# Performance work log

Measured on AMD Instinct MI355X. Metric: run time of the kernel, lower is better.

The kernel has to match this reference:

```python
import jax, jax.numpy as jnp
import numpy as np

B, C, L, MID, HID, OUT, K = 4096, 6, 1024, 512, 512, 256, 5
EPS = 1e-5


def _bn_eval(x, g, b, m, v):
    # BatchNorm1d eval mode on (B, C, T): normalize per channel with running stats
    inv = g / jnp.sqrt(v + EPS)
    return (x - m[None, :, None]) * inv[None, :, None] + b[None, :, None]


def setup_inputs() -> dict:
    key = jax.random.key(0)
    ks = jax.random.split(key, 12)
    s_in = 1.0 / np.sqrt(L)
    s_hid = 1.0 / np.sqrt(HID)
    inp = {
        "x": jax.random.normal(ks[0], (B, C, L), jnp.float32),
        # k stacked self-attention branches (two Linear(L, MID) each)
        "aW1": jax.random.normal(ks[1], (K, L, MID), jnp.float32) * s_in,
        "ab1": jnp.zeros((K, MID), jnp.float32),
        "aW2": jax.random.normal(ks[2], (K, L, MID), jnp.float32) * s_in,
        "ab2": jnp.zeros((K, MID), jnp.float32),
        # linearExchangeLayer: Linear(K*C, C)
        "linW": jax.random.normal(ks[3], (K * C, C), jnp.float32) / np.sqrt(K * C),
        "linb": jnp.zeros((C,), jnp.float32),
        # GraphConvolution weights
        "gW1": jax.random.normal(ks[4], (L, HID), jnp.float32) * s_in,
        "gb1": jnp.zeros((HID,), jnp.float32),
        "gW2": jax.random.normal(ks[5], (HID, OUT), jnp.float32) * s_hid,
        "gb2": jnp.zeros((OUT,), jnp.float32),
        # PReLU (single shared parameter, torch default 0.25)
        "prelu_a": jnp.array(0.25, jnp.float32),
        # BatchNorm1d params + running stats (eval mode)
        "bn1_g": jnp.ones((C,), jnp.float32),
        "bn1_b": jnp.zeros((C,), jnp.float32),
        "bn1_m": jnp.zeros((C,), jnp.float32),
        "bn1_v": jnp.ones((C,), jnp.float32),
        "bn2_g": jnp.ones((C,), jnp.float32),
        "bn2_b": jnp.zeros((C,), jnp.float32),
        "bn2_m": jnp.zeros((C,), jnp.float32),
        "bn2_v": jnp.ones((C,), jnp.float32),
    }
    return inp


def reference(x, aW1, ab1, aW2, ab2, linW, linb, gW1, gb1, gW2, gb2,
              prelu_a, bn1_g, bn1_b, bn1_m, bn1_v, bn2_g, bn2_b, bn2_m, bn2_v):
    b, c, l = x.shape
    k = aW1.shape[0]
    # --- multi-head attention adjacency: (b, c, c) ---
    q = jnp.einsum('bcl,klm->bkcm', x, aW1) + ab1[None, :, None, :]
    kv = jnp.einsum('bcl,klm->bkcm', x, aW2) + ab2[None, :, None, :]
    scores = jax.nn.softmax(jnp.einsum('bkcm,bkdm->bkcd', q, kv), axis=-1)
    # concat heads along last dim: (b, c, k*c)
    cat = scores.transpose(0, 2, 1, 3).reshape(b, c, k * c)
    A = jax.nn.softmax(cat @ linW + linb, axis=-1)  # (b, c, c)
    # --- GraphConvolution 1 (dropout identity in eval) ---
    h = jnp.einsum('bcd,bdh->bch', A, x @ gW1) + gb1
    # PReLU then BatchNorm1d
    h = jnp.where(h >= 0, h, prelu_a * h)
    h = _bn_eval(h, bn1_g, bn1_b, bn1_m, bn1_v)
    # --- GraphConvolution 2 ---
    out = jnp.einsum('bcd,bdh->bch', A, h @ gW2) + gb2
    out = _bn_eval(out, bn2_g, bn2_b, bn2_m, bn2_v)
    return out
```

## Files before the change

### kernel.cpp

```cpp
#include <hip/hip_runtime.h>
#include <hip/hip_bf16.h>


using bf16 = __hip_bfloat16;
using s16x8 = __attribute__((ext_vector_type(8))) short;
using f32x4 = __attribute__((ext_vector_type(4))) float;

#define AS1(p) ((__attribute__((address_space(1))) void*)((void*)(p)))
#define AS3(p) ((__attribute__((address_space(3))) void*)(p))

#if defined(__has_builtin)
#if __has_builtin(__builtin_amdgcn_global_load_lds)
#define HAVE_GLL 1
#endif
#endif

__device__ __forceinline__ float s2f(short s) {
  union { unsigned int u; float f; } c;
  c.u = ((unsigned int)(unsigned short)s) << 16;
  return c.f;
}
__device__ __forceinline__ short f2s(float x) {
  bf16 b = __float2bfloat16(x);
  short s;
  __builtin_memcpy(&s, &b, 2);
  return s;
}

__global__ void cvt_f32_bf16(const float* __restrict__ in, bf16* __restrict__ out, int n8) {
  int i = blockIdx.x * blockDim.x + threadIdx.x;
  if (i >= n8) return;
  float4 p0 = ((const float4*)in)[i * 2];
  float4 p1 = ((const float4*)in)[i * 2 + 1];
  s16x8 v;
  v[0] = f2s(p0.x); v[1] = f2s(p0.y); v[2] = f2s(p0.z); v[3] = f2s(p0.w);
  v[4] = f2s(p1.x); v[5] = f2s(p1.y); v[6] = f2s(p1.z); v[7] = f2s(p1.w);
  ((s16x8*)out)[i] = v;
}

__global__ void transpose_f2b(const float* __restrict__ in, bf16* __restrict__ out,
                              int R, int C) {
  __shared__ short tile[32][33];
  const float* src = in + (size_t)blockIdx.z * R * C;
  short* dst = (short*)out + (size_t)blockIdx.z * R * C;
  int r0 = blockIdx.x * 32, c0 = blockIdx.y * 32;
  int tx = threadIdx.x, ty = threadIdx.y;
#pragma unroll
  for (int i = 0; i < 4; ++i)
    tile[ty + i * 8][tx] = f2s(src[(size_t)(r0 + ty + i * 8) * C + c0 + tx]);
  __syncthreads();
#pragma unroll
  for (int i = 0; i < 4; ++i)
    dst[(size_t)(c0 + ty + i * 8) * R + r0 + tx] = tile[tx][ty + i * 8];
}

template <int AF32>
__global__ __launch_bounds__(256) void gemm_bt(
    const void* __restrict__ Ag,
    const bf16* __restrict__ Bt0, const bf16* __restrict__ Bt1,
    const float* __restrict__ bias0, const float* __restrict__ bias1, int boff,
    bf16* __restrict__ out0, bf16* __restrict__ out1,
    int M, int N, int K) {
  const bf16* Bt = (blockIdx.z == 0) ? Bt0 : Bt1;
  const float* bias = (blockIdx.z == 0) ? bias0 : bias1;
  bf16* Cg = (blockIdx.z == 0) ? out0 : out1;

  __shared__ short lA[128 * 32];
  __shared__ short lB[128 * 32];

  const int tid = threadIdx.x;
  const int lane = tid & 63, w = tid >> 6;
  const int wr = w >> 1, wc = w & 1;
  const int l16 = lane & 15, quad = lane >> 4;
  const int lrow = lane >> 2;
  const int scol = (((lane & 3) ^ ((lane >> 3) & 3)) * 8);

  const size_t rm0 = (size_t)blockIdx.x * 128;
  const size_t cn0 = (size_t)blockIdx.y * 128;

  f32x4 acc[4][4];
#pragma unroll
  for (int i = 0; i < 4; ++i)
#pragma unroll
    for (int j = 0; j < 4; ++j) acc[i][j] = (f32x4){0.f, 0.f, 0.f, 0.f};

  for (int kb = 0; kb < K; kb += 32) {
#pragma unroll
    for (int t = 0; t < 2; ++t) {
      int chunk = w * 2 + t;
      int row = chunk * 16 + lrow;
      const bf16* gb = Bt + (cn0 + row) * (size_t)K + kb + scol;
#ifdef HAVE_GLL
      __builtin_amdgcn_global_load_lds(AS1(gb), AS3(lB + chunk * 512), 16, 0, 0);
#else
      *(s16x8*)(lB + chunk * 512 + lane * 8) = *(const s16x8*)gb;
#endif
      if (AF32) {
        const float* ga = (const float*)Ag + (rm0 + row) * (size_t)K + kb + scol;
        float4 p0 = *(const float4*)ga;
        float4 p1 = *(const float4*)(ga + 4);
        s16x8 v;
        v[0] = f2s(p0.x); v[1] = f2s(p0.y); v[2] = f2s(p0.z); v[3] = f2s(p0.w);
        v[4] = f2s(p1.x); v[5] = f2s(p1.y); v[6] = f2s(p1.z); v[7] = f2s(p1.w);
        *(s16x8*)(lA + chunk * 512 + lane * 8) = v;
      } else {
        const bf16* ga = (const bf16*)Ag + (rm0 + row) * (size_t)K + kb + scol;
#ifdef HAVE_GLL
        __builtin_amdgcn_global_load_lds(AS1(ga), AS3(lA + chunk * 512), 16, 0, 0);
#else
        *(s16x8*)(lA + chunk * 512 + lane * 8) = *(const s16x8*)ga;
#endif
      }
    }
    __syncthreads();

    const int q2 = (quad ^ ((l16 >> 1) & 3)) * 8;
    s16x8 af[4], bfv[4];
#pragma unroll
    for (int i = 0; i < 4; ++i) {
      af[i] = *(const s16x8*)(lA + (wr * 64 + i * 16 + l16) * 32 + q2);
      bfv[i] = *(const s16x8*)(lB + (wc * 64 + i * 16 + l16) * 32 + q2);
    }
#pragma unroll
    for (int i = 0; i < 4; ++i)
#pragma unroll
      for (int j = 0; j < 4; ++j)
        acc[i][j] = __builtin_amdgcn_mfma_f32_16x16x32_bf16(af[i], bfv[j], acc[i][j], 0, 0, 0);
    __syncthreads();
  }

#pragma unroll
  for (int j = 0; j < 4; ++j) {
    size_t col = cn0 + wc * 64 + j * 16 + l16;
    float bv = bias ? bias[boff + col] : 0.f;
#pragma unroll
    for (int i = 0; i < 4; ++i) {
      size_t rowb = rm0 + wr * 64 + i * 16 + quad * 4;
#pragma unroll
      for (int r = 0; r < 4; ++r) {
        float v = acc[i][j][r] + bv;
        Cg[(rowb + r) * (size_t)N + col] = __float2bfloat16(v);
      }
    }
  }
}

__global__ __launch_bounds__(512, 2) void gemm256_8ph(
    const bf16* __restrict__ A,
    const bf16* __restrict__ Bt0, const bf16* __restrict__ Bt1,
    const float* __restrict__ bias0, const float* __restrict__ bias1, int boff,
    bf16* __restrict__ out0, bf16* __restrict__ out1,
    int M, int N, int K) {
  const bf16* Bt = (blockIdx.z == 0) ? Bt0 : Bt1;
  const float* bias = (blockIdx.z == 0) ? bias0 : bias1;
  bf16* Cg = (blockIdx.z == 0) ? out0 : out1;

  __shared__ __attribute__((aligned(16))) short ldsS[65536];

  const int tid = threadIdx.x;
  const int w = tid >> 6, l = tid & 63;
  const int l16 = l & 15, quad = l >> 4;
  const int wr = w >> 2, wc = w & 3;

  const size_t rm0 = (size_t)blockIdx.x * 256;
  const size_t cn0 = (size_t)blockIdx.y * 256;

  const int colS = ((l & 7) ^ (l >> 3)) * 8;
  const int rowS = w * 16 + (l >> 3);
  const short* pAs = (const short*)A + (rm0 + rowS) * (size_t)K + colS;
  const short* pBs = (const short*)Bt + (cn0 + rowS) * (size_t)K + colS;

  const int u0 = (quad ^ (l16 & 7)) * 8;
  const int u1 = ((quad + 4) ^ (l16 & 7)) * 8;

  f32x4 acc[8][4];
#pragma unroll
  for (int i = 0; i < 8; ++i)
#pragma unroll
    for (int j = 0; j < 4; ++j) acc[i][j] = (f32x4){0.f, 0.f, 0.f, 0.f};

  s16x8 af[4][2], bf0[2][2], bf1[2][2];

  const int T = K >> 6;

#ifdef HAVE_GLL
#define SA(BUF, H, KB) do {                                                          \
    __builtin_amdgcn_global_load_lds(AS1(pAs + (size_t)((H) * 128) * K + (KB)),      \
        AS3(ldsS + (BUF) * 32768 + (H) * 8192 + w * 1024), 16, 0, 0);                \
    __builtin_amdgcn_global_load_lds(AS1(pAs + (size_t)((H) * 128 + 8) * K + (KB)),  \
        AS3(ldsS + (BUF) * 32768 + (H) * 8192 + w * 1024 + 512), 16, 0, 0);          \
  } while (0)
#define SB(BUF, H, KB) do {                                                          \
    __builtin_amdgcn_global_load_lds(AS1(pBs + (size_t)((H) * 128) * K + (KB)),      \
        AS3(ldsS + (BUF) * 32768 + 16384 + (H) * 8192 + w * 1024), 16, 0, 0);        \
    __builtin_amdgcn_global_load_lds(AS1(pBs + (size_t)((H) * 128 + 8) * K + (KB)),  \
        AS3(ldsS + (BUF) * 32768 + 16384 + (H) * 8192 + w * 1024 + 512), 16, 0, 0);  \
  } while (0)
#else
#define SA(BUF, H, KB) do {                                                          \
    *(s16x8*)(ldsS + (BUF) * 32768 + (H) * 8192 + w * 1024 + l * 8) =                \
        *(const s16x8*)(pAs + (size_t)((H) * 128) * K + (KB));                       \
    *(s16x8*)(ldsS + (BUF) * 32768 + (H) * 8192 + w * 1024 + 512 + l * 8) =          \
        *(const s16x8*)(pAs + (size_t)((H) * 128 + 8) * K + (KB));                   \
  } while (0)
#define SB(BUF, H, KB) do {                                                          \
    *(s16x8*)(ldsS + (BUF) * 32768 + 16384 + (H) * 8192 + w * 1024 + l * 8) =        \
        *(const s16x8*)(pBs + (size_t)((H) * 128) * K + (KB));                       \
    *(s16x8*)(ldsS + (BUF) * 32768 + 16384 + (H) * 8192 + w * 1024 + 512 + l * 8) =  \
        *(const s16x8*)(pBs + (size_t)((H) * 128 + 8) * K + (KB));                   \
  } while (0)
#endif

#define LDA(BUF, MH) do {                                                            \
    _Pragma("unroll") for (int i = 0; i < 4; ++i) {                                  \
      const short* bse = ldsS + (BUF) * 32768 + wr * 8192 + (MH) * 4096 +            \
                         i * 1024 + l16 * 64;                                        \
      af[i][0] = *(const s16x8*)(bse + u0);                                          \
      af[i][1] = *(const s16x8*)(bse + u1);                                          \
    }                                                                                \
  } while (0)

#define LDB(BUF, NH, DST) do {                                                       \
    _Pragma("unroll") for (int n = 0; n < 2; ++n) {                                  \
      const short* bse = ldsS + (BUF) * 32768 + 16384 + (wc >> 1) * 8192 +           \
                         (wc & 1) * 4096 + (NH) * 2048 + n * 1024 + l16 * 64;        \
      DST[n][0] = *(const s16x8*)(bse + u0);                                         \
      DST[n][1] = *(const s16x8*)(bse + u1);                                         \
    }                                                                                \
  } while (0)

#define MFMAQ(MH, NH, BSET) do {                                                     \
    _Pragma("unroll") for (int i = 0; i < 4; ++i)                                    \
      _Pragma("unroll") for (int n = 0; n < 2; ++n) {                                \
        acc[(MH) * 4 + i][(NH) * 2 + n] = __builtin_amdgcn_mfma_f32_16x16x32_bf16(   \
            af[i][0], BSET[n][0], acc[(MH) * 4 + i][(NH) * 2 + n], 0, 0, 0);         \
        acc[(MH) * 4 + i][(NH) * 2 + n] = __builtin_amdgcn_mfma_f32_16x16x32_bf16(   \
            af[i][1], BSET[n][1], acc[(MH) * 4 + i][(NH) * 2 + n], 0, 0, 0);         \
      }                                                                              \
  } while (0)

#define BARX() asm volatile("s_barrier" ::: "memory")
#define LGKM0() do { asm volatile("s_waitcnt lgkmcnt(0)" ::: "memory");              \
                     __builtin_amdgcn_sched_barrier(0); } while (0)
#define VM6() do { asm volatile("s_waitcnt vmcnt(6)" ::: "memory");                  \
                   __builtin_amdgcn_sched_barrier(0); } while (0)

#define TILE_STEP(BUF, t) do {                                                       \
    const int kN_ = ((t) + 1 < T ? (t) + 1 : T - 1) << 6;                            \
    const int k2_ = ((t) + 2 < T ? (t) + 2 : T - 1) << 6;                            \
               \
    LDA(BUF, 0); LDB(BUF, 0, bf0); LDB(BUF, 1, bf1);                                 \
    SA((BUF) ^ 1, 1, kN_);                                                           \
    BARX(); LGKM0();                                                                 \
    __builtin_amdgcn_s_setprio(1); MFMAQ(0, 0, bf0); __builtin_amdgcn_s_setprio(0);  \
    BARX();                                                                          \
                        \
    SB(BUF, 0, k2_);                                                                 \
    BARX();                                                                          \
    __builtin_amdgcn_s_setprio(1); MFMAQ(0, 1, bf1); __builtin_amdgcn_s_setprio(0);  \
    BARX();                                                                          \
                                               \
    LDA(BUF, 1);                                                                     \
    SB(BUF, 1, k2_);                                                                 \
    BARX(); LGKM0();                                                                 \
    __builtin_amdgcn_s_setprio(1); MFMAQ(1, 1, bf1); __builtin_amdgcn_s_setprio(0);  \
    BARX();                                                                          \
                         \
    SA(BUF, 0, k2_);                                                                 \
    VM6();                                                                           \
    BARX();                                                                          \
    __builtin_amdgcn_s_setprio(1); MFMAQ(1, 0, bf0); __builtin_amdgcn_s_setprio(0);  \
    BARX();                                                                          \
  } while (0)

  {
    const int k1_ = (T > 1 ? 1 : 0) << 6;
    SB(0, 0, 0); SB(0, 1, 0); SA(0, 0, 0); SA(0, 1, 0);
    SB(1, 0, k1_); SB(1, 1, k1_); SA(1, 0, k1_);
    VM6();
    BARX();
  }

  for (int t = 0; t < T; t += 2) {
    TILE_STEP(0, t);
    TILE_STEP(1, t + 1);
  }

#pragma unroll
  for (int j = 0; j < 4; ++j) {
    size_t col = cn0 + wc * 64 + j * 16 + l16;
    float bv = bias ? bias[boff + col] : 0.f;
#pragma unroll
    for (int i = 0; i < 8; ++i) {
      size_t rowb = rm0 + wr * 128 + i * 16 + quad * 4;
#pragma unroll
      for (int r = 0; r < 4; ++r) {
        Cg[(rowb + r) * (size_t)N + col] = __float2bfloat16(acc[i][j][r] + bv);
      }
    }
  }
#undef SA
#undef SB
#undef LDA
#undef LDB
#undef MFMAQ
#undef BARX
#undef LGKM0
#undef VM6
#undef TILE_STEP
}

__global__ __launch_bounds__(256) void scores_mfma(
    const bf16* __restrict__ Q, const bf16* __restrict__ KV,
    float* __restrict__ S, int head) {
  const int tid = threadIdx.x;
  const int lane = tid & 63, w = tid >> 6;
  const int l16 = lane & 15, quad = lane >> 4;
  const int b0 = (blockIdx.x * 4 + w) * 2;

  int gr = (l16 < 8) ? (b0 * 6 + l16) : ((b0 + 1) * 6 + (l16 - 8));
  if (gr > 24575) gr = 24575;

  const short* qrow = (const short*)Q + (size_t)gr * 512 + quad * 8;
  const short* krow = (const short*)KV + (size_t)gr * 512 + quad * 8;

  f32x4 acc = (f32x4){0.f, 0.f, 0.f, 0.f};
#pragma unroll
  for (int kk = 0; kk < 16; ++kk) {
    s16x8 a = *(const s16x8*)(qrow + kk * 32);
    s16x8 b = *(const s16x8*)(krow + kk * 32);
    acc = __builtin_amdgcn_mfma_f32_16x16x32_bf16(a, b, acc, 0, 0, 0);
  }

  if (l16 < 6) {
#pragma unroll
    for (int r = 0; r < 4; ++r) {
      int m = quad * 4 + r;
      if (m < 6)
        S[((size_t)b0 * 5 + head) * 36 + m * 6 + l16] = acc[r];
    }
  } else if (l16 >= 8 && l16 < 14) {
#pragma unroll
    for (int r = 0; r < 4; ++r) {
      int m = quad * 4 + r;
      if (m >= 8 && m < 14)
        S[((size_t)(b0 + 1) * 5 + head) * 36 + (m - 8) * 6 + (l16 - 8)] = acc[r];
    }
  }
}

__global__ void batch_mid_kernel(const float* __restrict__ S, const bf16* __restrict__ XG,
                                 const float* __restrict__ linW, const float* __restrict__ linb,
                                 const float* __restrict__ gb1, const float* __restrict__ prelu,
                                 const float* __restrict__ g1, const float* __restrict__ b1,
                                 const float* __restrict__ m1, const float* __restrict__ v1,
                                 float* __restrict__ Afull, bf16* __restrict__ H) {
  int b = blockIdx.x, tid = threadIdx.x;
  __shared__ float p[5][6][6];
  __shared__ float Ar[6][6];
  __shared__ float lw[30][6];
  __shared__ float lbv[6];
  __shared__ float sc1[6], sm1[6], sb1[6];

  if (tid < 30) {
    int k = tid / 6, c = tid % 6;
    const float* sp = S + ((size_t)b * 5 + k) * 36 + c * 6;
    float v[6], mx = sp[0];
#pragma unroll
    for (int d = 0; d < 6; ++d) { v[d] = sp[d]; mx = fmaxf(mx, v[d]); }
    float s = 0.f;
#pragma unroll
    for (int d = 0; d < 6; ++d) { v[d] = expf(v[d] - mx); s += v[d]; }
    float inv = 1.f / s;
#pragma unroll
    for (int d = 0; d < 6; ++d) p[k][c][d] = v[d] * inv;
#pragma unroll
    for (int j = 0; j < 6; ++j) lw[tid][j] = linW[tid * 6 + j];
  }
  if (tid < 6) {
    lbv[tid] = linb[tid];
    sc1[tid] = g1[tid] * rsqrtf(v1[tid] + 1e-5f);
    sm1[tid] = m1[tid];
    sb1[tid] = b1[tid];
  }
  __syncthreads();

  if (tid < 6) {
    int c = tid;
    float ap[6];
#pragma unroll
    for (int j = 0; j < 6; ++j) ap[j] = lbv[j];
    for (int k = 0; k < 5; ++k)
#pragma unroll
      for (int d = 0; d < 6; ++d) {
        float pv = p[k][c][d];
#pragma unroll
        for (int j = 0; j < 6; ++j) ap[j] += pv * lw[k * 6 + d][j];
      }
    float mx = ap[0];
#pragma unroll
    for (int j = 1; j < 6; ++j) mx = fmaxf(mx, ap[j]);
    float s = 0.f;
#pragma unroll
    for (int j = 0; j < 6; ++j) { ap[j] = expf(ap[j] - mx); s += ap[j]; }
    float inv = 1.f / s;
#pragma unroll
    for (int j = 0; j < 6; ++j) {
      float a = ap[j] * inv;
      Ar[c][j] = a;
      Afull[(size_t)b * 36 + c * 6 + j] = a;
    }
  }
  __syncthreads();

  float pa = prelu[0];
  for (int col = tid; col < 512; col += 64) {
    float xg[6];
#pragma unroll
    for (int d = 0; d < 6; ++d) xg[d] = s2f(((const short*)XG)[((size_t)b * 6 + d) * 512 + col]);
    float gbv = gb1[col];
#pragma unroll
    for (int c = 0; c < 6; ++c) {
      float h = gbv;
#pragma unroll
      for (int d = 0; d < 6; ++d) h += Ar[c][d] * xg[d];
      h = (h >= 0.f) ? h : pa * h;
      h = (h - sm1[c]) * sc1[c] + sb1[c];
      H[((size_t)b * 6 + c) * 512 + col] = __float2bfloat16(h);
    }
  }
}

__global__ void batch_out_kernel(const float* __restrict__ Afull, const bf16* __restrict__ HW,
                                 const float* __restrict__ gb2,
                                 const float* __restrict__ g2, const float* __restrict__ b2,
                                 const float* __restrict__ m2, const float* __restrict__ v2,
                                 float* __restrict__ out) {
  int b = blockIdx.x, tid = threadIdx.x;
  __shared__ float Ar[36];
  __shared__ float sc[6], sm[6], sb[6];
  if (tid < 36) Ar[tid] = Afull[(size_t)b * 36 + tid];
  if (tid < 6) {
    sc[tid] = g2[tid] * rsqrtf(v2[tid] + 1e-5f);
    sm[tid] = m2[tid];
    sb[tid] = b2[tid];
  }
  __syncthreads();
  for (int col = tid; col < 256; col += 64) {
    float hw[6];
#pragma unroll
    for (int d = 0; d < 6; ++d) hw[d] = s2f(((const short*)HW)[((size_t)b * 6 + d) * 256 + col]);
    float gv = gb2[col];
#pragma unroll
    for (int c = 0; c < 6; ++c) {
      float o = gv;
#pragma unroll
      for (int d = 0; d < 6; ++d) o += Ar[c * 6 + d] * hw[d];
      o = (o - sm[c]) * sc[c] + sb[c];
      out[((size_t)b * 6 + c) * 256 + col] = o;
    }
  }
}

extern "C" void kernel_launch(void* const* d_in, const int* in_sizes, int n_in,
                              void* d_out, int out_size, void* d_ws, size_t ws_size,
                              hipStream_t stream) {
  const float* x    = (const float*)d_in[0];
  const float* aW1  = (const float*)d_in[1];
  const float* ab1  = (const float*)d_in[2];
  const float* aW2  = (const float*)d_in[3];
  const float* ab2  = (const float*)d_in[4];
  const float* linW = (const float*)d_in[5];
  const float* linb = (const float*)d_in[6];
  const float* gW1  = (const float*)d_in[7];
  const float* gb1  = (const float*)d_in[8];
  const float* gW2  = (const float*)d_in[9];
  const float* gb2  = (const float*)d_in[10];
  const float* prelu = (const float*)d_in[11];
  const float* bn1g = (const float*)d_in[12];
  const float* bn1b = (const float*)d_in[13];
  const float* bn1m = (const float*)d_in[14];
  const float* bn1v = (const float*)d_in[15];
  const float* bn2g = (const float*)d_in[16];
  const float* bn2b = (const float*)d_in[17];
  const float* bn2m = (const float*)d_in[18];
  const float* bn2v = (const float*)d_in[19];

  char* ws = (char*)d_ws;
  bf16* W1T  = (bf16*)(ws + 0);
  bf16* W2T  = (bf16*)(ws + 5242880);
  bf16* G1T  = (bf16*)(ws + 10485760);
  bf16* G2T  = (bf16*)(ws + 11534336);
  float* S   = (float*)(ws + 11796480);
  float* Af  = (float*)(ws + 14745600);
  bf16* BufA = (bf16*)(ws + 15335424);
  bf16* BufB = (bf16*)(ws + 40501248);
  bf16* Xb   = (bf16*)(ws + 65667072);
  const bool big = ws_size >= 115998720ull;

  dim3 tb(32, 8);
  transpose_f2b<<<dim3(32, 16, 5), tb, 0, stream>>>(aW1, W1T, 1024, 512);
  transpose_f2b<<<dim3(32, 16, 5), tb, 0, stream>>>(aW2, W2T, 1024, 512);
  transpose_f2b<<<dim3(32, 16, 1), tb, 0, stream>>>(gW1, G1T, 1024, 512);
  transpose_f2b<<<dim3(16, 8, 1),  tb, 0, stream>>>(gW2, G2T, 512, 256);
  if (big) cvt_f32_bf16<<<12288, 256, 0, stream>>>(x, Xb, 3145728);

  for (int k = 0; k < 5; ++k) {
    const bf16* w1 = W1T + (size_t)k * 512 * 1024;
    const bf16* w2 = W2T + (size_t)k * 512 * 1024;
    if (big)
      gemm256_8ph<<<dim3(96, 2, 2), 512, 0, stream>>>(
          Xb, w1, w2, ab1, ab2, k * 512, BufA, BufB, 24576, 512, 1024);
    else
      gemm_bt<1><<<dim3(192, 4, 2), 256, 0, stream>>>(
          x, w1, w2, ab1, ab2, k * 512, BufA, BufB, 24576, 512, 1024);
    scores_mfma<<<512, 256, 0, stream>>>(BufA, BufB, S, k);
  }

  if (big)
    gemm256_8ph<<<dim3(96, 2, 1), 512, 0, stream>>>(
        Xb, G1T, G1T, nullptr, nullptr, 0, BufA, BufA, 24576, 512, 1024);
  else
    gemm_bt<1><<<dim3(192, 4, 1), 256, 0, stream>>>(
        x, G1T, G1T, nullptr, nullptr, 0, BufA, BufA, 24576, 512, 1024);

  batch_mid_kernel<<<4096, 64, 0, stream>>>(S, BufA, linW, linb, gb1, prelu,
                                            bn1g, bn1b, bn1m, bn1v, Af, BufB);

  if (big)
    gemm256_8ph<<<dim3(96, 1, 1), 512, 0, stream>>>(
        BufB, G2T, G2T, nullptr, nullptr, 0, BufA, BufA, 24576, 256, 512);
  else
    gemm_bt<0><<<dim3(192, 2, 1), 256, 0, stream>>>(
        BufB, G2T, G2T, nullptr, nullptr, 0, BufA, BufA, 24576, 256, 512);

  batch_out_kernel<<<4096, 64, 0, stream>>>(Af, BufA, gb2, bn2g, bn2b, bn2m, bn2v,
                                            (float*)d_out);
}
```

Before: 678.5 us.

## Batch two attention heads per GEMM launch and fold the graph-conv GEMM in

Adds extra workspace buffers so two heads' Q/KV projections run in one gemm256_8ph launch (grid z=4), and the last head shares a launch with the X@gW1 GEMM. The scores kernel gains a second grid dimension to handle two heads at once. This cuts the number of launches and gives each launch more blocks to fill the GPU, at the cost of more workspace and a larger write footprint. The final G2 GEMM also moves from the 256-tile kernel to gemm_bt<0>.

```diff
diff --git a/kernel.cpp b/kernel.cpp
--- a/kernel.cpp
+++ b/kernel.cpp
@@ -26,6 +26,13 @@
   __builtin_memcpy(&s, &b, 2);
   return s;
 }
+
+struct GJob {
+  const bf16* Bt;
+  const float* bias;
+  int boff;
+  bf16* out;
+};
 
 __global__ void cvt_f32_bf16(const float* __restrict__ in, bf16* __restrict__ out, int n8) {
   int i = blockIdx.x * blockDim.x + threadIdx.x;
@@ -147,13 +154,14 @@
 
 __global__ __launch_bounds__(512, 2) void gemm256_8ph(
     const bf16* __restrict__ A,
-    const bf16* __restrict__ Bt0, const bf16* __restrict__ Bt1,
-    const float* __restrict__ bias0, const float* __restrict__ bias1, int boff,
-    bf16* __restrict__ out0, bf16* __restrict__ out1,
+    GJob j0, GJob j1, GJob j2, GJob j3,
     int M, int N, int K) {
-  const bf16* Bt = (blockIdx.z == 0) ? Bt0 : Bt1;
-  const float* bias = (blockIdx.z == 0) ? bias0 : bias1;
-  bf16* Cg = (blockIdx.z == 0) ? out0 : out1;
+  const GJob j = (blockIdx.z == 0) ? j0 : (blockIdx.z == 1) ? j1
+               : (blockIdx.z == 2) ? j2 : j3;
+  const bf16* Bt = j.Bt;
+  const float* bias = j.bias;
+  const int boff = j.boff;
+  bf16* Cg = j.out;
 
   __shared__ __attribute__((aligned(16))) short ldsS[65536];
 
@@ -177,7 +185,7 @@
 #pragma unroll
   for (int i = 0; i < 8; ++i)
 #pragma unroll
-    for (int j = 0; j < 4; ++j) acc[i][j] = (f32x4){0.f, 0.f, 0.f, 0.f};
+    for (int j2i = 0; j2i < 4; ++j2i) acc[i][j2i] = (f32x4){0.f, 0.f, 0.f, 0.f};
 
   s16x8 af[4][2], bf0[2][2], bf1[2][2];
 
@@ -287,15 +295,15 @@
   }
 
 #pragma unroll
-  for (int j = 0; j < 4; ++j) {
-    size_t col = cn0 + wc * 64 + j * 16 + l16;
+  for (int jj = 0; jj < 4; ++jj) {
+    size_t col = cn0 + wc * 64 + jj * 16 + l16;
     float bv = bias ? bias[boff + col] : 0.f;
 #pragma unroll
     for (int i = 0; i < 8; ++i) {
       size_t rowb = rm0 + wr * 128 + i * 16 + quad * 4;
 #pragma unroll
       for (int r = 0; r < 4; ++r) {
-        Cg[(rowb + r) * (size_t)N + col] = __float2bfloat16(acc[i][j][r] + bv);
+        Cg[(rowb + r) * (size_t)N + col] = __float2bfloat16(acc[i][jj][r] + bv);
       }
     }
   }
@@ -310,9 +318,15 @@
 #undef TILE_STEP
 }
 
-__global__ __launch_bounds__(256) void scores_mfma(
-    const bf16* __restrict__ Q, const bf16* __restrict__ KV,
-    float* __restrict__ S, int head) {
+__global__ __launch_bounds__(256) void scores_mfma2(
+    const bf16* __restrict__ Q0, const bf16* __restrict__ KV0,
+    const bf16* __restrict__ Q1, const bf16* __restrict__ KV1,
+    float* __restrict__ S, int head0) {
+  const int h = blockIdx.y;
+  const bf16* Q = h ? Q1 : Q0;
+  const bf16* KV = h ? KV1 : KV0;
+  const int head = head0 + h;
+
   const int tid = threadIdx.x;
   const int lane = tid & 63, w = tid >> 6;
   const int l16 = lane & 15, quad = lane >> 4;
@@ -496,7 +510,10 @@
   bf16* BufA = (bf16*)(ws + 15335424);
   bf16* BufB = (bf16*)(ws + 40501248);
   bf16* Xb   = (bf16*)(ws + 65667072);
-  const bool big = ws_size >= 115998720ull;
+  bf16* BufA2 = (bf16*)(ws + 115998720);
+  bf16* BufB2 = (bf16*)(ws + 141164544);
+  const bool big  = ws_size >= 115998720ull;
+  const bool big2 = ws_size >= 166330368ull;
 
   dim3 tb(32, 8);
   transpose_f2b<<<dim3(32, 16, 5), tb, 0, stream>>>(aW1, W1T, 1024, 512);
@@ -505,34 +522,57 @@
   transpose_f2b<<<dim3(16, 8, 1),  tb, 0, stream>>>(gW2, G2T, 512, 256);
   if (big) cvt_f32_bf16<<<12288, 256, 0, stream>>>(x, Xb, 3145728);
 
-  for (int k = 0; k < 5; ++k) {
-    const bf16* w1 = W1T + (size_t)k * 512 * 1024;
-    const bf16* w2 = W2T + (size_t)k * 512 * 1024;
-    if (big)
-      gemm256_8ph<<<dim3(96, 2, 2), 512, 0, stream>>>(
-          Xb, w1, w2, ab1, ab2, k * 512, BufA, BufB, 24576, 512, 1024);
-    else
-      gemm_bt<1><<<dim3(192, 4, 2), 256, 0, stream>>>(
-          x, w1, w2, ab1, ab2, k * 512, BufA, BufB, 24576, 512, 1024);
-    scores_mfma<<<512, 256, 0, stream>>>(BufA, BufB, S, k);
-  }
-
-  if (big)
-    gemm256_8ph<<<dim3(96, 2, 1), 512, 0, stream>>>(
-        Xb, G1T, G1T, nullptr, nullptr, 0, BufA, BufA, 24576, 512, 1024);
-  else
-    gemm_bt<1><<<dim3(192, 4, 1), 256, 0, stream>>>(
-        x, G1T, G1T, nullptr, nullptr, 0, BufA, BufA, 24576, 512, 1024);
-
-  batch_mid_kernel<<<4096, 64, 0, stream>>>(S, BufA, linW, linb, gb1, prelu,
-                                            bn1g, bn1b, bn1m, bn1v, Af, BufB);
-
-  if (big)
-    gemm256_8ph<<<dim3(96, 1, 1), 512, 0, stream>>>(
-        BufB, G2T, G2T, nullptr, nullptr, 0, BufA, BufA, 24576, 256, 512);
-  else
-    gemm_bt<0><<<dim3(192, 2, 1), 256, 0, stream>>>(
-        BufB, G2T, G2T, nullptr, nullptr, 0, BufA, BufA, 24576, 256, 512);
+  if (big2) {
+    for (int k = 0; k < 4; k += 2) {
+      const size_t wo0 = (size_t)k * 524288, wo1 = (size_t)(k + 1) * 524288;
+      GJob jq0{W1T + wo0, ab1, k * 512, BufA};
+      GJob jk0{W2T + wo0, ab2, k * 512, BufB};
+      GJob jq1{W1T + wo1, ab1, (k + 1) * 512, BufA2};
+      GJob jk1{W2T + wo1, ab2, (k + 1) * 512, BufB2};
+      gemm256_8ph<<<dim3(96, 2, 4), 512, 0, stream>>>(
+          Xb, jq0, jk0, jq1, jk1, 24576, 512, 1024);
+      scores_mfma2<<<dim3(512, 2), 256, 0, stream>>>(BufA, BufB, BufA2, BufB2, S, k);
+    }
+    {
+      const size_t wo4 = (size_t)4 * 524288;
+      GJob jq4{W1T + wo4, ab1, 4 * 512, BufA};
+      GJob jk4{W2T + wo4, ab2, 4 * 512, BufB};
+      GJob jxg{G1T, nullptr, 0, BufA2};
+      gemm256_8ph<<<dim3(96, 2, 3), 512, 0, stream>>>(
+          Xb, jq4, jk4, jxg, jxg, 24576, 512, 1024);
+      scores_mfma2<<<dim3(512, 1), 256, 0, stream>>>(BufA, BufB, BufA, BufB, S, 4);
+    }
+    batch_mid_kernel<<<4096, 64, 0, stream>>>(S, BufA2, linW, linb, gb1, prelu,
+                                              bn1g, bn1b, bn1m, bn1v, Af, BufB);
+  } else {
+    for (int k = 0; k < 5; ++k) {
+      const bf16* w1 = W1T + (size_t)k * 524288;
+      const bf16* w2 = W2T + (size_t)k * 524288;
+      if (big) {
+        GJob jq{w1, ab1, k * 512, BufA};
+        GJob jk{w2, ab2, k * 512, BufB};
+        gemm256_8ph<<<dim3(96, 2, 2), 512, 0, stream>>>(
+            Xb, jq, jk, jq, jk, 24576, 512, 1024);
+      } else {
+        gemm_bt<1><<<dim3(192, 4, 2), 256, 0, stream>>>(
+            x, w1, w2, ab1, ab2, k * 512, BufA, BufB, 24576, 512, 1024);
+      }
+      scores_mfma2<<<dim3(512, 1), 256, 0, stream>>>(BufA, BufB, BufA, BufB, S, k);
+    }
+    if (big) {
+      GJob jxg{G1T, nullptr, 0, BufA};
+      gemm256_8ph<<<dim3(96, 2, 1), 512, 0, stream>>>(
+          Xb, jxg, jxg, jxg, jxg, 24576, 512, 1024);
+    } else {
+      gemm_bt<1><<<dim3(192, 4, 1), 256, 0, stream>>>(
+          x, G1T, G1T, nullptr, nullptr, 0, BufA, BufA, 24576, 512, 1024);
+    }
+    batch_mid_kernel<<<4096, 64, 0, stream>>>(S, BufA, linW, linb, gb1, prelu,
+                                              bn1g, bn1b, bn1m, bn1v, Af, BufB);
+  }
+
+  gemm_bt<0><<<dim3(192, 2, 1), 256, 0, stream>>>(
+      BufB, G2T, G2T, nullptr, nullptr, 0, BufA, BufA, 24576, 256, 512);
 
   batch_out_kernel<<<4096, 64, 0, stream>>>(Af, BufA, gb2, bn2g, bn2b, bn2m, bn2v,
                                             (float*)d_out);
```

Result: faster. 631.5 us (-6.9%).
